# Kernel tuning notes

Measured on AMD Instinct MI355X. Metric: run time of the kernel, lower is better.

## Reference

```python
import jax, jax.numpy as jnp
import numpy as np

NUM_EMBEDDINGS = 1024
EMBEDDING_DIM = 256
COMMITMENT_COST = 0.25


def setup_inputs() -> dict:
    key = jax.random.key(0)
    k1, k2 = jax.random.split(key)
    inputs = jax.random.normal(k1, (32, EMBEDDING_DIM, 32, 32), dtype=jnp.float32)
    # torch init: uniform_(-1/K, 1/K)
    emb_w = jax.random.uniform(k2, (NUM_EMBEDDINGS, EMBEDDING_DIM), dtype=jnp.float32,
                               minval=-1.0 / NUM_EMBEDDINGS, maxval=1.0 / NUM_EMBEDDINGS)
    return {"inputs": inputs, "emb_w": emb_w}


def reference(inputs, emb_w):
    sg = jax.lax.stop_gradient
    # BCHW -> BHWC
    x = jnp.transpose(inputs, (0, 2, 3, 1))
    in_shape = x.shape
    flat = x.reshape(-1, EMBEDDING_DIM)  # [N, D]
    # squared L2 distances to codebook: [N, K]
    distances = (jnp.sum(flat * flat, axis=1, keepdims=True)
                 + jnp.sum(emb_w * emb_w, axis=1)
                 - 2.0 * jnp.matmul(flat, emb_w.T))
    idx = jnp.argmin(distances, axis=1)  # [N]
    encodings = jax.nn.one_hot(idx, NUM_EMBEDDINGS, dtype=jnp.float32)  # [N, K]
    # one-hot @ codebook == gather
    quantized = jnp.take(emb_w, idx, axis=0).reshape(in_shape)  # [B,H,W,D]
    e_latent_loss = jnp.mean((sg(quantized) - x) ** 2)
    q_latent_loss = jnp.mean((quantized - sg(x)) ** 2)
    loss = q_latent_loss + COMMITMENT_COST * e_latent_loss
    # straight-through estimator
    quantized_st = x + sg(quantized - x)
    avg_probs = jnp.mean(encodings, axis=0)
    perplexity = jnp.exp(-jnp.sum(avg_probs * jnp.log(avg_probs + 1e-10)))
    return (loss, jnp.transpose(quantized_st, (0, 3, 1, 2)), perplexity, encodings)
```

## Files before the change

### kernel.cpp

```cpp
#include <hip/hip_runtime.h>
#include <hip/hip_bf16.h>

typedef short short8 __attribute__((ext_vector_type(8)));
typedef float f32x4 __attribute__((ext_vector_type(4)));
typedef unsigned short u16x4 __attribute__((ext_vector_type(4)));

#define D_ 256
#define K_ 1024
#define HW_ 1024
#define NROWS_ 32768
#define QELEMS 8388608
#define NBLK_ (NROWS_ / 64)

static __device__ __forceinline__ unsigned short to_bf16(float v) {
    __hip_bfloat16 h = __float2bfloat16(v);
    return *(unsigned short*)&h;
}

__global__ __launch_bounds__(256) void vq_prep(const float* __restrict__ emb,
    unsigned short* __restrict__ ebf, float* __restrict__ enorm,
    int* __restrict__ counts, double* __restrict__ loss_acc, int* __restrict__ done)
{
    int k = blockIdx.x, t = threadIdx.x;
    float v = emb[k * D_ + t];
    ebf[k * D_ + t] = to_bf16(v);
    float s = v * v;
    for (int o = 32; o > 0; o >>= 1) s += __shfl_down(s, o);
    __shared__ float ws4[4];
    if ((t & 63) == 0) ws4[t >> 6] = s;
    __syncthreads();
    if (t == 0) enorm[k] = ws4[0] + ws4[1] + ws4[2] + ws4[3];
    if (k < 4) counts[k * 256 + t] = 0;
    if (k == 0 && t == 0) { *loss_acc = 0.0; *done = 0; }
}

__global__ __launch_bounds__(512, 4) void vq_main(
    const float* __restrict__ x, const float* __restrict__ emb,
    const unsigned short* __restrict__ ebf, const float* __restrict__ enorm,
    int* __restrict__ counts, double* __restrict__ loss_acc, int* __restrict__ done,
    float* __restrict__ out)
{
    __shared__ char smem[65536];
    __shared__ float xn[64][9];
    __shared__ float ens[1024];
    __shared__ float rminv[64][4];
    __shared__ int   rmini[64][4];
    __shared__ int   bestsh[64];
    __shared__ double sred2[8];
    __shared__ int lastflag;

    unsigned short* xs = (unsigned short*)smem;
    char* es = smem;

    const int t = threadIdx.x;
    const int n0 = blockIdx.x * 64;
    const int b = n0 >> 10;
    const int hw0 = n0 & 1023;
    const float* xbase = x + (size_t)b * (D_ * HW_) + hw0;

    ens[t] = enorm[t];
    ens[t + 512] = enorm[t + 512];

    {
        const int rt = t & 15;
        const int r0 = rt * 4;
        const int dg = t >> 4;
        float xp[4] = {0.f, 0.f, 0.f, 0.f};
#pragma unroll
        for (int m = 0; m < 2; ++m) {
            int d0 = (dg + 32 * m) * 4;
            f32x4 c[4];
#pragma unroll
            for (int q = 0; q < 4; ++q)
                c[q] = *(const f32x4*)(xbase + (size_t)(d0 + q) * HW_ + r0);
#pragma unroll
            for (int i = 0; i < 4; ++i) {
                u16x4 pk;
                pk[0] = to_bf16(c[0][i]); pk[1] = to_bf16(c[1][i]);
                pk[2] = to_bf16(c[2][i]); pk[3] = to_bf16(c[3][i]);
                xp[i] = fmaf(c[0][i], c[0][i], xp[i]);
                xp[i] = fmaf(c[1][i], c[1][i], xp[i]);
                xp[i] = fmaf(c[2][i], c[2][i], xp[i]);
                xp[i] = fmaf(c[3][i], c[3][i], xp[i]);
                int r = r0 + i;
                int byte = (r * 512 + d0 * 2) ^ ((r & 7) << 4);
                *(u16x4*)((char*)xs + byte) = pk;
            }
        }
#pragma unroll
        for (int i = 0; i < 4; ++i) {
            xp[i] += __shfl_down(xp[i], 32);
            xp[i] += __shfl_down(xp[i], 16);
        }
        if ((t & 48) == 0) {
            int w0 = t >> 6;
#pragma unroll
            for (int i = 0; i < 4; ++i) xn[r0 + i][w0] = xp[i];
        }
    }
    __syncthreads();

    const int lane = t & 63;
    const int w = t >> 6;
    const int rh = w & 1;
    const int cq = w >> 1;
    const int col = lane & 15;
    const int kg = lane >> 4;
    const char* ebf_bytes = (const char*)ebf;
    const int wbyte = w * 4096;

    float2* ezw = (float2*)(out + 8388610 + (size_t)(n0 + w * 8) * 1024);
    const float2 zz2 = {0.f, 0.f};

    {
#pragma unroll
        for (int j = 0; j < 4; ++j) {
            int p = wbyte + j * 1024 + lane * 16;
            int qq = p ^ (((p >> 9) & 7) << 4);
            __builtin_amdgcn_global_load_lds(ebf_bytes + qq, es + 32768 + wbyte + j * 1024, 16, 0, 0);
        }
        __builtin_amdgcn_sched_barrier(0);
        float2* ez = ezw + 15 * 256;
#pragma unroll
        for (int j = 0; j < 4; ++j) ez[j * 64 + lane] = zz2;
        __builtin_amdgcn_sched_barrier(0);
    }

    short8 areg[2][8];
#pragma unroll
    for (int rt = 0; rt < 2; ++rt) {
        int row = rh * 32 + rt * 16 + col;
        int rowb = row * 512;
        int sw = (row & 7) << 4;
#pragma unroll
        for (int dc = 0; dc < 8; ++dc) {
            int byte = (rowb + dc * 64 + kg * 16) ^ sw;
            areg[rt][dc] = *(const short8*)((const char*)xs + byte);
        }
    }

    float v1[8]; int i1[8];
#pragma unroll
    for (int s = 0; s < 8; ++s) { v1[s] = 3.4e38f; i1[s] = 0x7fffffff; }

    for (int cc = 0; cc < 16; ++cc) {
        asm volatile("s_waitcnt vmcnt(4)" ::: "memory");
        __builtin_amdgcn_s_barrier();
        __builtin_amdgcn_sched_barrier(0);
        const int hc = ((cc & 1) ^ 1) * 32768;
        if (cc < 15) {
            const char* src = ebf_bytes + (size_t)(cc + 1) * 32768;
            const int hn = (cc & 1) * 32768;
#pragma unroll
            for (int j = 0; j < 4; ++j) {
                int p = wbyte + j * 1024 + lane * 16;
                int qq = p ^ (((p >> 9) & 7) << 4);
                __builtin_amdgcn_global_load_lds(src + qq, es + hn + wbyte + j * 1024, 16, 0, 0);
            }
            __builtin_amdgcn_sched_barrier(0);
            float2* ez = ezw + cc * 256;
#pragma unroll
            for (int j = 0; j < 4; ++j) ez[j * 64 + lane] = zz2;
            __builtin_amdgcn_sched_barrier(0);
        }
        const int c0 = cq * 16 + col;
        const int sw0 = (c0 & 7) << 4;
        f32x4 acc0 = {0.f, 0.f, 0.f, 0.f};
        f32x4 acc1 = {0.f, 0.f, 0.f, 0.f};
#pragma unroll
        for (int dc = 0; dc < 8; ++dc) {
            short8 bf = *(const short8*)(es + hc + ((c0 * 512 + dc * 64 + kg * 16) ^ sw0));
            acc0 = __builtin_amdgcn_mfma_f32_16x16x32_bf16(areg[0][dc], bf, acc0, 0, 0, 0);
            acc1 = __builtin_amdgcn_mfma_f32_16x16x32_bf16(areg[1][dc], bf, acc1, 0, 0, 0);
        }
        int code = cc * 64 + c0;
        float bn = ens[code];
#pragma unroll
        for (int r = 0; r < 4; ++r) {
            float dv = fmaf(-2.f, acc0[r], bn);
            if (dv < v1[r]) { v1[r] = dv; i1[r] = code; }
            float dw = fmaf(-2.f, acc1[r], bn);
            if (dw < v1[4 + r]) { v1[4 + r] = dw; i1[4 + r] = code; }
        }
    }

#pragma unroll
    for (int mask = 1; mask < 16; mask <<= 1) {
#pragma unroll
        for (int s = 0; s < 8; ++s) {
            float ov = __shfl_xor(v1[s], mask);
            int oi = __shfl_xor(i1[s], mask);
            if (ov < v1[s] || (ov == v1[s] && oi < i1[s])) { v1[s] = ov; i1[s] = oi; }
        }
    }
    if (col == 0) {
#pragma unroll
        for (int s = 0; s < 8; ++s) {
            int rt = s >> 2, r = s & 3;
            int row = rh * 32 + rt * 16 + kg * 4 + r;
            rminv[row][cq] = v1[s];
            rmini[row][cq] = i1[s];
        }
    }
    __syncthreads();

    if (t < 64) {
        float dmin = rminv[t][0]; int best = rmini[t][0];
#pragma unroll
        for (int g = 1; g < 4; ++g) {
            float cv = rminv[t][g]; int ci = rmini[t][g];
            if (cv < dmin || (cv == dmin && ci < best)) { dmin = cv; best = ci; }
        }
        bestsh[t] = best;
        atomicAdd(&counts[best], 1);
        float s = 0.f;
#pragma unroll
        for (int g = 0; g < 8; ++g) s += xn[t][g];
        float lrow = dmin + s;
        for (int o = 32; o > 0; o >>= 1) lrow += __shfl_down(lrow, o);
        if (t == 0) atomicAdd(loss_acc, (double)lrow);
    }
    __syncthreads();

    {
        int rr = lane >> 3;
        int r  = w * 8 + rr;
        int c  = lane & 7;
        const f32x4* src4 = (const f32x4*)emb + (size_t)bestsh[r] * 64;
        float* q = (float*)smem + r * 256;
        int xr = r & 31;
#pragma unroll
        for (int j = 0; j < 8; ++j) {
            f32x4 v = src4[8 * j + c];
#pragma unroll
            for (int k = 0; k < 4; ++k) {
                int d = 4 * (8 * j + c) + k;
                q[d ^ xr] = v[k];
            }
        }
    }
    __syncthreads();

    {
        const int hwr = t & 63;
        const int dq = t >> 6;
        float* outq = out + 1 + (size_t)b * (D_ * HW_) + hw0 + hwr;
        const float* q = (const float*)smem + hwr * 256;
        int xr = hwr & 31;
#pragma unroll
        for (int dd = 0; dd < 32; ++dd) {
            int d = dq + dd * 8;
            outq[(size_t)d * HW_] = q[d ^ xr];
        }
    }
    if (t < 64) out[8388610 + (size_t)(n0 + t) * 1024 + bestsh[t]] = 1.0f;
    __syncthreads();

    if (t == 0) {
        __threadfence();
        int old = atomicAdd(done, 1);
        lastflag = (old == NBLK_ - 1) ? 1 : 0;
    }
    __syncthreads();
    if (lastflag) {
        double s = 0.0;
#pragma unroll
        for (int j = 0; j < 2; ++j) {
            int k = t * 2 + j;
            int cnt = __hip_atomic_load(&counts[k], __ATOMIC_RELAXED, __HIP_MEMORY_SCOPE_AGENT);
            double p = (double)cnt / 32768.0;
            s += p * log(p + 1e-10);
        }
        for (int o = 32; o > 0; o >>= 1) s += __shfl_down(s, o);
        if (lane == 0) sred2[w] = s;
        __syncthreads();
        if (t == 0) {
            double tot = 0.0;
#pragma unroll
            for (int g = 0; g < 8; ++g) tot += sred2[g];
            double lw = __hip_atomic_load(loss_acc, __ATOMIC_RELAXED, __HIP_MEMORY_SCOPE_AGENT);
            out[0] = (float)(1.25 * lw / (double)QELEMS);
            out[8388609] = (float)exp(-tot);
        }
    }
}

extern "C" void kernel_launch(void* const* d_in, const int* in_sizes, int n_in,
                              void* d_out, int out_size, void* d_ws, size_t ws_size,
                              hipStream_t stream)
{
    const float* x = (const float*)d_in[0];
    const float* emb = (const float*)d_in[1];
    char* ws = (char*)d_ws;
    unsigned short* ebf = (unsigned short*)(ws);
    float* enorm = (float*)(ws + 524288);
    int* counts = (int*)(ws + 528384);
    double* lacc = (double*)(ws + 532480);
    int* done = (int*)(ws + 532488);
    float* out = (float*)d_out;

    vq_prep<<<K_, 256, 0, stream>>>(emb, ebf, enorm, counts, lacc, done);
    vq_main<<<NBLK_, 512, 0, stream>>>(x, emb, ebf, enorm, counts, lacc, done, out);
}
```

Measured before the change: 74.93 us.

## Pre-tile bf16 codebook into MFMA fragment order and defer one-hot zeroing

The prep kernel now writes the bf16 codebook in a tiled layout that matches the MFMA B-fragment order, and the x tile in LDS uses the same fragment-major layout. Each lane then loads operands with a contiguous lane*16 offset, so the XOR swizzle arithmetic goes away. The prep launch shrinks to 64 blocks, and codebook norms are read from global memory instead of being staged in LDS. The one-hot zero stores are no longer interleaved with the main loop; they run after it, which gives up their overlap with the MFMA work and risks a burst of write traffic afterward.

Result: slower. 120.2 us (+60.4%).

```diff
diff --git a/kernel.cpp b/kernel.cpp
--- a/kernel.cpp
+++ b/kernel.cpp
@@ -18,38 +18,57 @@
 }
 
 __global__ __launch_bounds__(256) void vq_prep(const float* __restrict__ emb,
-    unsigned short* __restrict__ ebf, float* __restrict__ enorm,
+    unsigned short* __restrict__ ebf2, float* __restrict__ enorm,
     int* __restrict__ counts, double* __restrict__ loss_acc, int* __restrict__ done)
 {
-    int k = blockIdx.x, t = threadIdx.x;
-    float v = emb[k * D_ + t];
-    ebf[k * D_ + t] = to_bf16(v);
-    float s = v * v;
-    for (int o = 32; o > 0; o >>= 1) s += __shfl_down(s, o);
-    __shared__ float ws4[4];
-    if ((t & 63) == 0) ws4[t >> 6] = s;
-    __syncthreads();
-    if (t == 0) enorm[k] = ws4[0] + ws4[1] + ws4[2] + ws4[3];
-    if (k < 4) counts[k * 256 + t] = 0;
-    if (k == 0 && t == 0) { *loss_acc = 0.0; *done = 0; }
+    __shared__ float part[256];
+    const int ct = blockIdx.x, t = threadIdx.x;
+    const int col = t & 15, s = t >> 4;
+    const int k = ct * 16 + col;
+    const f32x4* src = (const f32x4*)(emb + (size_t)k * D_ + s * 16);
+    short8 f0, f1;
+    float a = 0.f;
+#pragma unroll
+    for (int j = 0; j < 4; ++j) {
+        f32x4 v = src[j];
+#pragma unroll
+        for (int q = 0; q < 4; ++q) {
+            int idx = j * 4 + q;
+            unsigned short h = to_bf16(v[q]);
+            a = fmaf(v[q], v[q], a);
+            if (idx < 8) f0[idx] = (short)h; else f1[idx - 8] = (short)h;
+        }
+    }
+    part[t] = a;
+    char* base = (char*)ebf2 + ct * 8192 + (s >> 1) * 1024 + ((s & 1) * 2) * 256 + col * 16;
+    *(short8*)base = f0;
+    *(short8*)(base + 256) = f1;
+    __syncthreads();
+    if (t < 16) {
+        float s2 = 0.f;
+#pragma unroll
+        for (int j = 0; j < 16; ++j) s2 += part[t + 16 * j];
+        enorm[ct * 16 + t] = s2;
+    }
+    if (ct < 4) counts[ct * 256 + t] = 0;
+    if (ct == 0 && t == 0) { *loss_acc = 0.0; *done = 0; }
 }
 
 __global__ __launch_bounds__(512, 4) void vq_main(
     const float* __restrict__ x, const float* __restrict__ emb,
-    const unsigned short* __restrict__ ebf, const float* __restrict__ enorm,
+    const unsigned short* __restrict__ ebf2, const float* __restrict__ enorm,
     int* __restrict__ counts, double* __restrict__ loss_acc, int* __restrict__ done,
     float* __restrict__ out)
 {
     __shared__ char smem[65536];
     __shared__ float xn[64][9];
-    __shared__ float ens[1024];
     __shared__ float rminv[64][4];
     __shared__ int   rmini[64][4];
     __shared__ int   bestsh[64];
     __shared__ double sred2[8];
     __shared__ int lastflag;
 
-    unsigned short* xs = (unsigned short*)smem;
+    char* xs = smem;
     char* es = smem;
 
     const int t = threadIdx.x;
@@ -58,12 +77,8 @@
     const int hw0 = n0 & 1023;
     const float* xbase = x + (size_t)b * (D_ * HW_) + hw0;
 
-    ens[t] = enorm[t];
-    ens[t + 512] = enorm[t + 512];
-
-    {
-        const int rt = t & 15;
-        const int r0 = rt * 4;
+    {
+        const int rt = t & 15, r0 = rt * 4;
         const int dg = t >> 4;
         float xp[4] = {0.f, 0.f, 0.f, 0.f};
 #pragma unroll
@@ -73,6 +88,7 @@
 #pragma unroll
             for (int q = 0; q < 4; ++q)
                 c[q] = *(const f32x4*)(xbase + (size_t)(d0 + q) * HW_ + r0);
+            const int dc = d0 >> 5, kg = (d0 >> 3) & 3, off = (d0 & 7) * 2;
 #pragma unroll
             for (int i = 0; i < 4; ++i) {
                 u16x4 pk;
@@ -83,8 +99,8 @@
                 xp[i] = fmaf(c[2][i], c[2][i], xp[i]);
                 xp[i] = fmaf(c[3][i], c[3][i], xp[i]);
                 int r = r0 + i;
-                int byte = (r * 512 + d0 * 2) ^ ((r & 7) << 4);
-                *(u16x4*)((char*)xs + byte) = pk;
+                int byte = ((r >> 4) << 13) + (dc << 10) + (kg << 8) + ((r & 15) << 4) + off;
+                *(u16x4*)(xs + byte) = pk;
             }
         }
 #pragma unroll
@@ -98,45 +114,29 @@
             for (int i = 0; i < 4; ++i) xn[r0 + i][w0] = xp[i];
         }
     }
-    __syncthreads();
 
     const int lane = t & 63;
     const int w = t >> 6;
     const int rh = w & 1;
     const int cq = w >> 1;
     const int col = lane & 15;
-    const int kg = lane >> 4;
-    const char* ebf_bytes = (const char*)ebf;
+    const char* eb = (const char*)ebf2;
     const int wbyte = w * 4096;
 
-    float2* ezw = (float2*)(out + 8388610 + (size_t)(n0 + w * 8) * 1024);
-    const float2 zz2 = {0.f, 0.f};
-
-    {
-#pragma unroll
-        for (int j = 0; j < 4; ++j) {
-            int p = wbyte + j * 1024 + lane * 16;
-            int qq = p ^ (((p >> 9) & 7) << 4);
-            __builtin_amdgcn_global_load_lds(ebf_bytes + qq, es + 32768 + wbyte + j * 1024, 16, 0, 0);
-        }
-        __builtin_amdgcn_sched_barrier(0);
-        float2* ez = ezw + 15 * 256;
-#pragma unroll
-        for (int j = 0; j < 4; ++j) ez[j * 64 + lane] = zz2;
-        __builtin_amdgcn_sched_barrier(0);
-    }
+    __syncthreads();
+
+#pragma unroll
+    for (int j = 0; j < 4; ++j)
+        __builtin_amdgcn_global_load_lds(eb + wbyte + j * 1024 + lane * 16,
+                                         es + 32768 + wbyte + j * 1024, 16, 0, 0);
 
     short8 areg[2][8];
 #pragma unroll
     for (int rt = 0; rt < 2; ++rt) {
-        int row = rh * 32 + rt * 16 + col;
-        int rowb = row * 512;
-        int sw = (row & 7) << 4;
-#pragma unroll
-        for (int dc = 0; dc < 8; ++dc) {
-            int byte = (rowb + dc * 64 + kg * 16) ^ sw;
-            areg[rt][dc] = *(const short8*)((const char*)xs + byte);
-        }
+        const char* ab = xs + ((rh * 2 + rt) << 13);
+#pragma unroll
+        for (int dc = 0; dc < 8; ++dc)
+            areg[rt][dc] = *(const short8*)(ab + dc * 1024 + lane * 16);
     }
 
     float v1[8]; int i1[8];
@@ -144,37 +144,27 @@
     for (int s = 0; s < 8; ++s) { v1[s] = 3.4e38f; i1[s] = 0x7fffffff; }
 
     for (int cc = 0; cc < 16; ++cc) {
-        asm volatile("s_waitcnt vmcnt(4)" ::: "memory");
-        __builtin_amdgcn_s_barrier();
-        __builtin_amdgcn_sched_barrier(0);
+        __syncthreads();
         const int hc = ((cc & 1) ^ 1) * 32768;
         if (cc < 15) {
-            const char* src = ebf_bytes + (size_t)(cc + 1) * 32768;
+            const char* src = eb + (size_t)(cc + 1) * 32768;
             const int hn = (cc & 1) * 32768;
 #pragma unroll
-            for (int j = 0; j < 4; ++j) {
-                int p = wbyte + j * 1024 + lane * 16;
-                int qq = p ^ (((p >> 9) & 7) << 4);
-                __builtin_amdgcn_global_load_lds(src + qq, es + hn + wbyte + j * 1024, 16, 0, 0);
-            }
-            __builtin_amdgcn_sched_barrier(0);
-            float2* ez = ezw + cc * 256;
-#pragma unroll
-            for (int j = 0; j < 4; ++j) ez[j * 64 + lane] = zz2;
-            __builtin_amdgcn_sched_barrier(0);
-        }
-        const int c0 = cq * 16 + col;
-        const int sw0 = (c0 & 7) << 4;
+            for (int j = 0; j < 4; ++j)
+                __builtin_amdgcn_global_load_lds(src + wbyte + j * 1024 + lane * 16,
+                                                 es + hn + wbyte + j * 1024, 16, 0, 0);
+        }
+        const char* tb = es + hc + (cq << 13);
         f32x4 acc0 = {0.f, 0.f, 0.f, 0.f};
         f32x4 acc1 = {0.f, 0.f, 0.f, 0.f};
 #pragma unroll
         for (int dc = 0; dc < 8; ++dc) {
-            short8 bf = *(const short8*)(es + hc + ((c0 * 512 + dc * 64 + kg * 16) ^ sw0));
+            short8 bf = *(const short8*)(tb + dc * 1024 + lane * 16);
             acc0 = __builtin_amdgcn_mfma_f32_16x16x32_bf16(areg[0][dc], bf, acc0, 0, 0, 0);
             acc1 = __builtin_amdgcn_mfma_f32_16x16x32_bf16(areg[1][dc], bf, acc1, 0, 0, 0);
         }
-        int code = cc * 64 + c0;
-        float bn = ens[code];
+        const int code = cc * 64 + cq * 16 + col;
+        const float bn = enorm[code];
 #pragma unroll
         for (int r = 0; r < 4; ++r) {
             float dv = fmaf(-2.f, acc0[r], bn);
@@ -184,6 +174,13 @@
         }
     }
 
+    {
+        float2* ez = (float2*)(out + 8388610 + (size_t)(n0 + w * 8) * 1024);
+        const float2 zz = {0.f, 0.f};
+#pragma unroll 8
+        for (int j = 0; j < 64; ++j) ez[j * 64 + lane] = zz;
+    }
+
 #pragma unroll
     for (int mask = 1; mask < 16; mask <<= 1) {
 #pragma unroll
@@ -193,13 +190,16 @@
             if (ov < v1[s] || (ov == v1[s] && oi < i1[s])) { v1[s] = ov; i1[s] = oi; }
         }
     }
-    if (col == 0) {
-#pragma unroll
-        for (int s = 0; s < 8; ++s) {
-            int rt = s >> 2, r = s & 3;
-            int row = rh * 32 + rt * 16 + kg * 4 + r;
-            rminv[row][cq] = v1[s];
-            rmini[row][cq] = i1[s];
+    {
+        const int kg = lane >> 4;
+        if (col == 0) {
+#pragma unroll
+            for (int s = 0; s < 8; ++s) {
+                int rt = s >> 2, r = s & 3;
+                int row = rh * 32 + rt * 16 + kg * 4 + r;
+                rminv[row][cq] = v1[s];
+                rmini[row][cq] = i1[s];
+            }
         }
     }
     __syncthreads();
@@ -223,9 +223,8 @@
     __syncthreads();
 
     {
-        int rr = lane >> 3;
-        int r  = w * 8 + rr;
-        int c  = lane & 7;
+        int r = w * 8 + (lane >> 3);
+        int c = lane & 7;
         const f32x4* src4 = (const f32x4*)emb + (size_t)bestsh[r] * 64;
         float* q = (float*)smem + r * 256;
         int xr = r & 31;
@@ -233,9 +232,9 @@
         for (int j = 0; j < 8; ++j) {
             f32x4 v = src4[8 * j + c];
 #pragma unroll
-            for (int k = 0; k < 4; ++k) {
-                int d = 4 * (8 * j + c) + k;
-                q[d ^ xr] = v[k];
+            for (int kq = 0; kq < 4; ++kq) {
+                int d = 4 * (8 * j + c) + kq;
+                q[d ^ xr] = v[kq];
             }
         }
     }
@@ -272,7 +271,7 @@
             s += p * log(p + 1e-10);
         }
         for (int o = 32; o > 0; o >>= 1) s += __shfl_down(s, o);
-        if (lane == 0) sred2[w] = s;
+        if ((t & 63) == 0) sred2[t >> 6] = s;
         __syncthreads();
         if (t == 0) {
             double tot = 0.0;
@@ -292,13 +291,13 @@
     const float* x = (const float*)d_in[0];
     const float* emb = (const float*)d_in[1];
     char* ws = (char*)d_ws;
-    unsigned short* ebf = (unsigned short*)(ws);
+    unsigned short* ebf2 = (unsigned short*)(ws);
     float* enorm = (float*)(ws + 524288);
     int* counts = (int*)(ws + 528384);
     double* lacc = (double*)(ws + 532480);
     int* done = (int*)(ws + 532488);
     float* out = (float*)d_out;
 
-    vq_prep<<<K_, 256, 0, stream>>>(emb, ebf, enorm, counts, lacc, done);
-    vq_main<<<NBLK_, 512, 0, stream>>>(x, emb, ebf, enorm, counts, lacc, done, out);
+    vq_prep<<<64, 256, 0, stream>>>(emb, ebf2, enorm, counts, lacc, done);
+    vq_main<<<NBLK_, 512, 0, stream>>>(x, emb, ebf2, enorm, counts, lacc, done, out);
 }
```
